# Kernel optimization log

Measured on AMD Instinct MI355X. Metric: run time of the kernel, lower is better.

Reference implementation:

```python
import jax, jax.numpy as jnp
import numpy as np

EMB = 512
HEADS = 8
HEAD_DIM = EMB // HEADS


def setup_inputs() -> dict:
    key = jax.random.key(0)
    ks = jax.random.split(key, 8)
    S, B = 2048, 2
    q = jax.random.normal(ks[0], (S, B, EMB), dtype=jnp.float32)
    k = jax.random.normal(ks[1], (S, B, EMB), dtype=jnp.float32)
    v = jax.random.normal(ks[2], (S, B, EMB), dtype=jnp.float32)
    sc = 1.0 / np.sqrt(HEAD_DIM)
    Wq = jax.random.normal(ks[3], (HEAD_DIM, HEAD_DIM), dtype=jnp.float32) * sc
    Wk = jax.random.normal(ks[4], (HEAD_DIM, HEAD_DIM), dtype=jnp.float32) * sc
    Wv = jax.random.normal(ks[5], (HEAD_DIM, HEAD_DIM), dtype=jnp.float32) * sc
    Wfc = jax.random.normal(ks[6], (EMB, EMB), dtype=jnp.float32) * (1.0 / np.sqrt(EMB))
    bfc = jax.random.normal(ks[7], (EMB,), dtype=jnp.float32) * 0.01
    return {"q": q, "k": k, "v": v, "Wq": Wq, "Wk": Wk, "Wv": Wv, "Wfc": Wfc, "bfc": bfc}


def reference(q, k, v, Wq, Wk, Wv, Wfc, bfc):
    query_len, batch, emb = q.shape
    key_len = k.shape[0]
    value_len = v.shape[0]
    # Faithful to the original: plain reshape (NOT transpose) from [S,B,E] -> [B,H,S,D]
    qh = q.reshape(batch, HEADS, query_len, HEAD_DIM)
    kh = k.reshape(batch, HEADS, key_len, HEAD_DIM)
    vh = v.reshape(batch, HEADS, value_len, HEAD_DIM)
    # torch Linear(head_dim, head_dim, bias=False): y = x @ W.T
    Q = qh @ Wq.T
    K = kh @ Wk.T
    V = vh @ Wv.T
    QK = jnp.einsum('bhqd,bhkd->bhqk', Q, K)  # [B,H,S,S] score matrix (memory-bound)
    filt = jax.nn.softmax(QK / np.sqrt(HEAD_DIM).astype(np.float32), axis=3)
    att = jnp.einsum('bhqk,bhkd->bhqd', filt, V)
    att = att.reshape(query_len, batch, emb)
    return att @ Wfc.T + bfc
```

## Files before the change

kernel.cpp:

```cpp
#include <hip/hip_runtime.h>
#include <hip/hip_bf16.h>


typedef __attribute__((ext_vector_type(8))) __bf16 bf16x8;
typedef __attribute__((ext_vector_type(4))) float f32x4;
typedef __attribute__((ext_vector_type(16))) float f32x16;
typedef __attribute__((ext_vector_type(4))) unsigned short u16x4;
typedef __attribute__((ext_vector_type(4))) unsigned int u32x4;
typedef unsigned short u16;
typedef unsigned int u32;

static __device__ __forceinline__ u16 f2bf(float x) {
    u32 u = __float_as_uint(x);
    u += 0x7fff + ((u >> 16) & 1);
    return (u16)(u >> 16);
}
static __device__ __forceinline__ float bf2f(u16 h) {
    return __uint_as_float(((u32)h) << 16);
}
static __device__ __forceinline__ u32 pk2(float lo, float hi) {
    __hip_bfloat162 h2 = __float22bfloat162_rn(make_float2(lo, hi));
    u32 r; __builtin_memcpy(&r, &h2, 4); return r;
}

__global__ __launch_bounds__(256) void proj_kernel(
    const float* __restrict__ q, const float* __restrict__ k, const float* __restrict__ v,
    const float* __restrict__ Wq, const float* __restrict__ Wk, const float* __restrict__ Wv,
    const float* __restrict__ Wfc,
    u16* __restrict__ Qb, u16* __restrict__ Kb, u16* __restrict__ Vt,
    u16* __restrict__ Wb, float* __restrict__ KnSq)
{
    const int mode = blockIdx.z;
    const int t = threadIdx.x;

    if (mode == 3) {
        int i = (blockIdx.x * 256 + t) * 4;
        float4 val = *(const float4*)(Wfc + i);
        uint2 b = { pk2(val.x, val.y), pk2(val.z, val.w) };
        *(uint2*)(Wb + i) = b;
        return;
    }

    const float* A = (mode == 0) ? q : (mode == 1) ? k : v;
    const float* W = (mode == 0) ? Wq : (mode == 1) ? Wk : Wv;
    const float osc = (mode == 0) ? 0.18033688011112042f : 1.0f;

    __shared__ alignas(16) u16 Ash[128 * 88];
    __shared__ alignas(16) u16 Wsh[64 * 88];
    __shared__ float red[128];

    const int m0 = blockIdx.x * 128;
    const int w = t >> 6, l = t & 63;
    const int r16 = l & 15, q4 = l >> 4;

    {
        const float4* A4 = (const float4*)(A + (size_t)m0 * 64);
        const int c4 = t & 15;
        #pragma unroll
        for (int i = 0; i < 8; ++i) {
            int row = (t >> 4) + i * 16;
            float4 val = A4[row * 16 + c4];
            uint2 bb = { pk2(val.x, val.y), pk2(val.z, val.w) };
            *(uint2*)(Ash + row * 88 + c4 * 4) = bb;
        }
        const float4* W4 = (const float4*)W;
        #pragma unroll
        for (int i = 0; i < 4; ++i) {
            int row = (t >> 4) + i * 16;
            float4 val = W4[row * 16 + c4];
            uint2 bb = { pk2(val.x, val.y), pk2(val.z, val.w) };
            *(uint2*)(Wsh + row * 88 + c4 * 4) = bb;
        }
    }
    __syncthreads();

    bf16x8 af[2][2], wf[4][2];
    #pragma unroll
    for (int mc = 0; mc < 2; ++mc)
        #pragma unroll
        for (int kk = 0; kk < 2; ++kk)
            af[mc][kk] = *(const bf16x8*)(Ash + (w * 32 + mc * 16 + r16) * 88 + kk * 32 + q4 * 8);
    #pragma unroll
    for (int nc = 0; nc < 4; ++nc)
        #pragma unroll
        for (int kk = 0; kk < 2; ++kk)
            wf[nc][kk] = *(const bf16x8*)(Wsh + (nc * 16 + r16) * 88 + kk * 32 + q4 * 8);

    f32x4 acc[2][4];
    const f32x4 zero = {0.f, 0.f, 0.f, 0.f};
    #pragma unroll
    for (int mc = 0; mc < 2; ++mc)
        #pragma unroll
        for (int nc = 0; nc < 4; ++nc) {
            acc[mc][nc] = __builtin_amdgcn_mfma_f32_16x16x32_bf16(af[mc][0], wf[nc][0], zero, 0, 0, 0);
            acc[mc][nc] = __builtin_amdgcn_mfma_f32_16x16x32_bf16(af[mc][1], wf[nc][1], acc[mc][nc], 0, 0, 0);
        }

    __syncthreads();

    if (mode < 2) {
        #pragma unroll
        for (int mc = 0; mc < 2; ++mc)
            #pragma unroll
            for (int nc = 0; nc < 4; ++nc)
                #pragma unroll
                for (int r = 0; r < 4; ++r)
                    Ash[(w * 32 + mc * 16 + q4 * 4 + r) * 72 + nc * 16 + r16] = f2bf(acc[mc][nc][r] * osc);
        __syncthreads();
        u16* Out = ((mode == 0) ? Qb : Kb) + (size_t)m0 * 64;
        {
            int row = t >> 1, cbase = (t & 1) * 32;
            #pragma unroll
            for (int i = 0; i < 4; ++i)
                *(u32x4*)(Out + row * 64 + cbase + i * 8) = *(const u32x4*)(Ash + row * 72 + cbase + i * 8);
        }
        if (mode == 1) {
            if (t < 128) {
                float ss = 0.f;
                #pragma unroll
                for (int c = 0; c < 8; ++c) {
                    u32x4 d = *(const u32x4*)(Ash + t * 72 + c * 8);
                    #pragma unroll
                    for (int j = 0; j < 4; ++j) {
                        float lo = bf2f((u16)(d[j] & 0xffff));
                        float hi = bf2f((u16)(d[j] >> 16));
                        ss += lo * lo + hi * hi;
                    }
                }
                red[t] = ss;
            }
            __syncthreads();
            if (t < 64) red[t] = fmaxf(red[t], red[t + 64]);
            __syncthreads();
            if (t < 32) red[t] = fmaxf(red[t], red[t + 32]);
            __syncthreads();
            if (t == 0) {
                float mx = red[0];
                for (int i = 1; i < 32; ++i) mx = fmaxf(mx, red[i]);
                KnSq[blockIdx.x] = mx;
            }
        }
    } else {
        #pragma unroll
        for (int mc = 0; mc < 2; ++mc)
            #pragma unroll
            for (int nc = 0; nc < 4; ++nc)
                #pragma unroll
                for (int r = 0; r < 4; ++r)
                    Ash[(nc * 16 + r16) * 136 + w * 32 + mc * 16 + q4 * 4 + r] = f2bf(acc[mc][nc][r]);
        __syncthreads();
        const int g = m0 >> 11, s0 = m0 & 2047;
        int d = t >> 2, sb = (t & 3) * 32;
        u16* Out = Vt + ((size_t)(g * 64 + d)) * 2048 + s0;
        #pragma unroll
        for (int i = 0; i < 4; ++i)
            *(u32x4*)(Out + sb + i * 8) = *(const u32x4*)(Ash + d * 136 + sb + i * 8);
    }
}

__global__ __launch_bounds__(256) void flash_kernel(
    const u16* __restrict__ Qb, const u16* __restrict__ Kb,
    const u16* __restrict__ Vt, const float* __restrict__ KnSq,
    u16* __restrict__ Att)
{
    const int bi = blockIdx.x;
    const int g = bi & 15;
    const int qt = bi >> 4;
    const int t = threadIdx.x, w = t >> 6, l = t & 63;
    const int q5 = l & 31, h = l >> 5;
    const int qs = w >> 1, kh = w & 1;

    __shared__ alignas(16) unsigned char smem[43008];
    u16* const base16 = (u16*)smem;
    u16* const KT0 = base16;
    u16* const KT1 = base16 + 4096;
    u16* const VS0 = base16 + 8192;
    u16* const VS1 = base16 + 12288;
    u16* const PwB = base16 + 16384 + w * 1280;

    const u16* Kg = Kb + ((size_t)g) * 2048 * 64;
    const u16* Vg = Vt + ((size_t)g) * 64 * 2048;

    bf16x8 qb[4];
    {
        const u16* qp = Qb + ((size_t)(g * 2048 + qt * 64 + qs * 32 + q5)) * 64;
        #pragma unroll
        for (int s = 0; s < 4; ++s)
            qb[s] = *(const bf16x8*)(qp + s * 16 + h * 8);
    }

    float m;
    {
        float kss = KnSq[g * 16 + (l & 15)];
        kss = fmaxf(kss, __shfl_xor(kss, 1));
        kss = fmaxf(kss, __shfl_xor(kss, 2));
        kss = fmaxf(kss, __shfl_xor(kss, 4));
        kss = fmaxf(kss, __shfl_xor(kss, 8));
        float ss = 0.f;
        #pragma unroll
        for (int s = 0; s < 4; ++s)
            #pragma unroll
            for (int j = 0; j < 8; ++j) {
                float x = (float)qb[s][j];
                ss += x * x;
            }
        ss += __shfl_xor(ss, 32);
        m = sqrtf(ss * kss) * 1.0002f;
    }

    const int rr = t >> 3, ck = t & 7;
    const int sw = (ck ^ (rr & 7)) * 8;

    {
        #pragma unroll
        for (int h2 = 0; h2 < 2; ++h2) {
            int row = h2 * 32 + rr;
            *(u32x4*)(KT0 + row * 64 + sw) = *(const u32x4*)(Kg + (size_t)row * 64 + ck * 8);
            *(u32x4*)(VS0 + row * 64 + sw) = *(const u32x4*)(Vg + (size_t)row * 2048 + ck * 8);
        }
    }
    __syncthreads();

    f32x16 z16;
    #pragma unroll
    for (int r = 0; r < 16; ++r) z16[r] = 0.f;
    f32x16 o0 = z16, o1 = z16;
    float psum = 0.f;

    const int rk = kh * 32 + q5;
    const int r7 = q5 & 7;
    u16* const pwRow = PwB + q5 * 40;
    const int vc0 = 4 * kh + h;
    const int vc1 = 4 * kh + 2 + h;

    for (int it = 0; it < 32; ++it) {
        u16* const KTc = (it & 1) ? KT1 : KT0;
        u16* const VSc = (it & 1) ? VS1 : VS0;
        u16* const KTn = (it & 1) ? KT0 : KT1;
        u16* const VSn = (it & 1) ? VS0 : VS1;
        const bool hasn = (it < 31);

        u32x4 knx[2], vnx[2];
        if (hasn) {
            #pragma unroll
            for (int h2 = 0; h2 < 2; ++h2) {
                int row = h2 * 32 + rr;
                knx[h2] = *(const u32x4*)(Kg + (size_t)((it + 1) * 64 + row) * 64 + ck * 8);
                vnx[h2] = *(const u32x4*)(Vg + (size_t)row * 2048 + (it + 1) * 64 + ck * 8);
            }
        }

        bf16x8 ka0 = *(const bf16x8*)(KTc + rk * 64 + (((0 + h) ^ r7) * 8));
        bf16x8 ka1 = *(const bf16x8*)(KTc + rk * 64 + (((2 + h) ^ r7) * 8));
        bf16x8 ka2 = *(const bf16x8*)(KTc + rk * 64 + (((4 + h) ^ r7) * 8));
        bf16x8 ka3 = *(const bf16x8*)(KTc + rk * 64 + (((6 + h) ^ r7) * 8));
        f32x16 s;
        s = __builtin_amdgcn_mfma_f32_32x32x16_bf16(ka0, qb[0], z16, 0, 0, 0);
        s = __builtin_amdgcn_mfma_f32_32x32x16_bf16(ka1, qb[1], s, 0, 0, 0);
        s = __builtin_amdgcn_mfma_f32_32x32x16_bf16(ka2, qb[2], s, 0, 0, 0);
        s = __builtin_amdgcn_mfma_f32_32x32x16_bf16(ka3, qb[3], s, 0, 0, 0);

        float p[16];
        float ps = 0.f;
        #pragma unroll
        for (int r = 0; r < 16; ++r) {
            p[r] = exp2f(s[r] - m);
            ps += p[r];
        }
        psum += ps;

        #pragma unroll
        for (int u = 0; u < 4; ++u) {
            uint2 dd = { pk2(p[4 * u + 0], p[4 * u + 1]),
                         pk2(p[4 * u + 2], p[4 * u + 3]) };
            *(uint2*)(pwRow + u * 8 + 4 * h) = dd;
        }
        bf16x8 pb0 = *(const bf16x8*)(pwRow + (0 + h) * 8);
        bf16x8 pb1 = *(const bf16x8*)(pwRow + (2 + h) * 8);

        {
            bf16x8 va0 = *(const bf16x8*)(VSc + q5 * 64 + ((vc0 ^ r7) * 8));
            bf16x8 va1 = *(const bf16x8*)(VSc + q5 * 64 + ((vc1 ^ r7) * 8));
            o0 = __builtin_amdgcn_mfma_f32_32x32x16_bf16(va0, pb0, o0, 0, 0, 0);
            o0 = __builtin_amdgcn_mfma_f32_32x32x16_bf16(va1, pb1, o0, 0, 0, 0);
        }
        {
            bf16x8 va0 = *(const bf16x8*)(VSc + (32 + q5) * 64 + ((vc0 ^ r7) * 8));
            bf16x8 va1 = *(const bf16x8*)(VSc + (32 + q5) * 64 + ((vc1 ^ r7) * 8));
            o1 = __builtin_amdgcn_mfma_f32_32x32x16_bf16(va0, pb0, o1, 0, 0, 0);
            o1 = __builtin_amdgcn_mfma_f32_32x32x16_bf16(va1, pb1, o1, 0, 0, 0);
        }

        if (hasn) {
            #pragma unroll
            for (int h2 = 0; h2 < 2; ++h2) {
                int row = h2 * 32 + rr;
                *(u32x4*)(KTn + row * 64 + sw) = knx[h2];
                *(u32x4*)(VSn + row * 64 + sw) = vnx[h2];
            }
        }
        __syncthreads();
    }

    float psq = psum + __shfl_xor(psum, 32);

    float* const Fsh = (float*)smem;
    float* const LsF = (float*)(smem + 16896);
    u16*  const Osh = (u16*)(smem + 18432);

    if (kh == 1) {
        float* fp = Fsh + (qs * 64 + l) * 33;
        #pragma unroll
        for (int r = 0; r < 16; ++r) { fp[r] = o0[r]; fp[16 + r] = o1[r]; }
        fp[32] = psq;
        LsF[qs * 64 + l] = psq;
    }
    __syncthreads();
    if (kh == 0) {
        const float* fp = Fsh + (qs * 64 + l) * 33;
        float inv = 1.0f / (psq + LsF[qs * 64 + l]);
        const int qloc = qs * 32 + q5;
        #pragma unroll
        for (int u = 0; u < 4; ++u) {
            uint2 b0 = { pk2((o0[4*u+0] + fp[4*u+0]) * inv, (o0[4*u+1] + fp[4*u+1]) * inv),
                         pk2((o0[4*u+2] + fp[4*u+2]) * inv, (o0[4*u+3] + fp[4*u+3]) * inv) };
            *(uint2*)(Osh + qloc * 72 + 8 * u + 4 * h) = b0;
            uint2 b1 = { pk2((o1[4*u+0] + fp[16+4*u+0]) * inv, (o1[4*u+1] + fp[16+4*u+1]) * inv),
                         pk2((o1[4*u+2] + fp[16+4*u+2]) * inv, (o1[4*u+3] + fp[16+4*u+3]) * inv) };
            *(uint2*)(Osh + qloc * 72 + 32 + 8 * u + 4 * h) = b1;
        }
    }
    __syncthreads();
    {
        int row = t >> 2, cb = (t & 3) * 16;
        u16* dst = Att + ((size_t)(g * 2048 + qt * 64 + row)) * 64 + cb;
        *(u32x4*)(dst)     = *(const u32x4*)(Osh + row * 72 + cb);
        *(u32x4*)(dst + 8) = *(const u32x4*)(Osh + row * 72 + cb + 8);
    }
}

__global__ __launch_bounds__(256) void fc_kernel(
    const u16* __restrict__ Att, const u16* __restrict__ Wb,
    const float* __restrict__ bfc, float* __restrict__ out)
{
    __shared__ alignas(16) u16 Ash[2][64 * 64];
    __shared__ alignas(16) u16 Wsh[2][64 * 64];

    const int t = threadIdx.x, w = t >> 6, l = t & 63;
    const int r16 = l & 15, q4 = l >> 4;
    const int r7 = r16 & 7;
    const int m0 = blockIdx.x * 64, n0 = blockIdx.y * 64;

    const int rr = t >> 3, ck = t & 7;
    const int sw0 = (ck ^ (rr & 7)) * 8;
    const int fr0 = (q4 ^ r7) * 8;
    const int fr1 = ((q4 + 4) ^ r7) * 8;

    {
        #pragma unroll
        for (int h = 0; h < 2; ++h) {
            int row = h * 32 + rr;
            *(u32x4*)(&Ash[0][row * 64 + sw0]) = *(const u32x4*)(Att + (size_t)(m0 + row) * 512 + ck * 8);
            *(u32x4*)(&Wsh[0][row * 64 + sw0]) = *(const u32x4*)(Wb + (size_t)(n0 + row) * 512 + ck * 8);
        }
    }
    __syncthreads();

    f32x4 acc[4];
    const f32x4 zero = {0.f, 0.f, 0.f, 0.f};
    #pragma unroll
    for (int nc = 0; nc < 4; ++nc) acc[nc] = zero;

    for (int it = 0; it < 8; ++it) {
        const int cur = it & 1;
        const bool hasn = (it < 7);

        u32x4 anx[2], wnx[2];
        if (hasn) {
            #pragma unroll
            for (int h = 0; h < 2; ++h) {
                int row = h * 32 + rr;
                anx[h] = *(const u32x4*)(Att + (size_t)(m0 + row) * 512 + (it + 1) * 64 + ck * 8);
                wnx[h] = *(const u32x4*)(Wb + (size_t)(n0 + row) * 512 + (it + 1) * 64 + ck * 8);
            }
        }

        bf16x8 af[2], wf[4][2];
        af[0] = *(const bf16x8*)(&Ash[cur][(w * 16 + r16) * 64 + fr0]);
        af[1] = *(const bf16x8*)(&Ash[cur][(w * 16 + r16) * 64 + fr1]);
        #pragma unroll
        for (int nc = 0; nc < 4; ++nc) {
            wf[nc][0] = *(const bf16x8*)(&Wsh[cur][(nc * 16 + r16) * 64 + fr0]);
            wf[nc][1] = *(const bf16x8*)(&Wsh[cur][(nc * 16 + r16) * 64 + fr1]);
        }

        #pragma unroll
        for (int nc = 0; nc < 4; ++nc) {
            acc[nc] = __builtin_amdgcn_mfma_f32_16x16x32_bf16(af[0], wf[nc][0], acc[nc], 0, 0, 0);
            acc[nc] = __builtin_amdgcn_mfma_f32_16x16x32_bf16(af[1], wf[nc][1], acc[nc], 0, 0, 0);
        }

        if (hasn) {
            const int nxt = cur ^ 1;
            #pragma unroll
            for (int h = 0; h < 2; ++h) {
                int row = h * 32 + rr;
                *(u32x4*)(&Ash[nxt][row * 64 + sw0]) = anx[h];
                *(u32x4*)(&Wsh[nxt][row * 64 + sw0]) = wnx[h];
            }
        }
        __syncthreads();
    }

    #pragma unroll
    for (int nc = 0; nc < 4; ++nc) {
        float bb = bfc[n0 + nc * 16 + r16];
        #pragma unroll
        for (int r = 0; r < 4; ++r) {
            int row = m0 + w * 16 + q4 * 4 + r;
            out[(size_t)row * 512 + n0 + nc * 16 + r16] = acc[nc][r] + bb;
        }
    }
}

extern "C" void kernel_launch(void* const* d_in, const int* in_sizes, int n_in,
                              void* d_out, int out_size, void* d_ws, size_t ws_size,
                              hipStream_t stream) {
    (void)in_sizes; (void)n_in; (void)out_size; (void)ws_size;
    const float* q   = (const float*)d_in[0];
    const float* k   = (const float*)d_in[1];
    const float* v   = (const float*)d_in[2];
    const float* Wq  = (const float*)d_in[3];
    const float* Wk  = (const float*)d_in[4];
    const float* Wv  = (const float*)d_in[5];
    const float* Wfc = (const float*)d_in[6];
    const float* bfc = (const float*)d_in[7];
    float* out = (float*)d_out;

    u16* Qb = (u16*)d_ws;
    u16* Kb = Qb + 2097152;
    u16* Vt = Kb + 2097152;
    u16* At = Vt + 2097152;
    u16* Wb = At + 2097152;
    float* KnSq = (float*)((char*)d_ws + 17301504);

    proj_kernel<<<dim3(256, 1, 4), 256, 0, stream>>>(q, k, v, Wq, Wk, Wv, Wfc,
                                                     Qb, Kb, Vt, Wb, KnSq);
    flash_kernel<<<dim3(512), 256, 0, stream>>>(Qb, Kb, Vt, KnSq, At);
    fc_kernel<<<dim3(64, 8), 256, 0, stream>>>(At, Wb, bfc, out);
}
```

Before: 138.3 us.

## Store Q/K/V in MFMA fragment layout and load K/V directly into registers

The projection kernel now writes Q, K and V in a pre-swizzled layout that matches the MFMA operand fragments. This lets the flash kernel load K/V tiles straight from global memory into registers with register double-buffering, removing the LDS staging and the per-iteration __syncthreads. It also folds the -m offset into the MFMA accumulator init and computes the row sum with an extra MFMA against a ones vector instead of scalar adds. In exchange, each wave redundantly fetches K/V from global/L2 instead of sharing them through LDS, and it uses more registers.

```diff
diff --git a/kernel.cpp b/kernel.cpp
--- a/kernel.cpp
+++ b/kernel.cpp
@@ -27,7 +27,7 @@
     const float* __restrict__ q, const float* __restrict__ k, const float* __restrict__ v,
     const float* __restrict__ Wq, const float* __restrict__ Wk, const float* __restrict__ Wv,
     const float* __restrict__ Wfc,
-    u16* __restrict__ Qb, u16* __restrict__ Kb, u16* __restrict__ Vt,
+    u16* __restrict__ Qf, u16* __restrict__ Kf, u16* __restrict__ Vf,
     u16* __restrict__ Wb, float* __restrict__ KnSq)
 {
     const int mode = blockIdx.z;
@@ -97,6 +97,8 @@
         }
 
     __syncthreads();
+
+    const int g = m0 >> 11, t0 = (m0 & 2047) >> 6;
 
     if (mode < 2) {
         #pragma unroll
@@ -107,12 +109,17 @@
                 for (int r = 0; r < 4; ++r)
                     Ash[(w * 32 + mc * 16 + q4 * 4 + r) * 72 + nc * 16 + r16] = f2bf(acc[mc][nc][r] * osc);
         __syncthreads();
-        u16* Out = ((mode == 0) ? Qb : Kb) + (size_t)m0 * 64;
-        {
-            int row = t >> 1, cbase = (t & 1) * 32;
-            #pragma unroll
-            for (int i = 0; i < 4; ++i)
-                *(u32x4*)(Out + row * 64 + cbase + i * 8) = *(const u32x4*)(Ash + row * 72 + cbase + i * 8);
+        u16* Out = (mode == 0) ? Qf : Kf;
+        #pragma unroll
+        for (int i = 0; i < 4; ++i) {
+            int idx = i * 256 + t;
+            int ll = idx & 63;
+            int r = idx >> 6;
+            int tl = r >> 3, c2 = (r >> 2) & 1, s = r & 3;
+            int row = tl * 64 + c2 * 32 + (ll & 31);
+            int col = s * 16 + (ll >> 5) * 8;
+            u32x4 d = *(const u32x4*)(Ash + row * 72 + col);
+            *(u32x4*)(Out + ((size_t)(((g * 32 + t0 + tl) * 2 + c2) * 4 + s) * 64 + ll) * 8) = d;
         }
         if (mode == 1) {
             if (t < 128) {
@@ -149,18 +156,23 @@
                 for (int r = 0; r < 4; ++r)
                     Ash[(nc * 16 + r16) * 136 + w * 32 + mc * 16 + q4 * 4 + r] = f2bf(acc[mc][nc][r]);
         __syncthreads();
-        const int g = m0 >> 11, s0 = m0 & 2047;
-        int d = t >> 2, sb = (t & 3) * 32;
-        u16* Out = Vt + ((size_t)(g * 64 + d)) * 2048 + s0;
-        #pragma unroll
-        for (int i = 0; i < 4; ++i)
-            *(u32x4*)(Out + sb + i * 8) = *(const u32x4*)(Ash + d * 136 + sb + i * 8);
+        #pragma unroll
+        for (int i = 0; i < 4; ++i) {
+            int idx = i * 256 + t;
+            int ll = idx & 63;
+            int r = idx >> 6;
+            int tl = r >> 3, kh = (r >> 2) & 1, dc = (r >> 1) & 1, s2 = r & 1;
+            int d = dc * 32 + (ll & 31);
+            int keycol = tl * 64 + kh * 32 + s2 * 16 + (ll >> 5) * 8;
+            u32x4 val = *(const u32x4*)(Ash + d * 136 + keycol);
+            *(u32x4*)(Vf + ((size_t)((((g * 32 + t0 + tl) * 2 + kh) * 2 + dc) * 2 + s2) * 64 + ll) * 8) = val;
+        }
     }
 }
 
 __global__ __launch_bounds__(256) void flash_kernel(
-    const u16* __restrict__ Qb, const u16* __restrict__ Kb,
-    const u16* __restrict__ Vt, const float* __restrict__ KnSq,
+    const u16* __restrict__ Qf, const u16* __restrict__ Kf,
+    const u16* __restrict__ Vf, const float* __restrict__ KnSq,
     u16* __restrict__ Att)
 {
     const int bi = blockIdx.x;
@@ -170,24 +182,16 @@
     const int q5 = l & 31, h = l >> 5;
     const int qs = w >> 1, kh = w & 1;
 
-    __shared__ alignas(16) unsigned char smem[43008];
-    u16* const base16 = (u16*)smem;
-    u16* const KT0 = base16;
-    u16* const KT1 = base16 + 4096;
-    u16* const VS0 = base16 + 8192;
-    u16* const VS1 = base16 + 12288;
-    u16* const PwB = base16 + 16384 + w * 1280;
-
-    const u16* Kg = Kb + ((size_t)g) * 2048 * 64;
-    const u16* Vg = Vt + ((size_t)g) * 64 * 2048;
+    __shared__ alignas(16) unsigned char smem[26624];
+    u16* const pwRow = (u16*)smem + w * 1280 + q5 * 40;
+
+    const u16* qbase = Qf + ((size_t)(((g * 32 + qt) * 2 + qs) * 4)) * 512 + l * 8;
+    const u16* kbase = Kf + ((size_t)((g * 32 * 2 + kh) * 4)) * 512 + l * 8;
+    const u16* vbase = Vf + ((size_t)((g * 32 * 2 + kh) * 4)) * 512 + l * 8;
 
     bf16x8 qb[4];
-    {
-        const u16* qp = Qb + ((size_t)(g * 2048 + qt * 64 + qs * 32 + q5)) * 64;
-        #pragma unroll
-        for (int s = 0; s < 4; ++s)
-            qb[s] = *(const bf16x8*)(qp + s * 16 + h * 8);
-    }
+    #pragma unroll
+    for (int s = 0; s < 4; ++s) qb[s] = *(const bf16x8*)(qbase + s * 512);
 
     float m;
     {
@@ -208,66 +212,37 @@
         m = sqrtf(ss * kss) * 1.0002f;
     }
 
-    const int rr = t >> 3, ck = t & 7;
-    const int sw = (ck ^ (rr & 7)) * 8;
-
-    {
-        #pragma unroll
-        for (int h2 = 0; h2 < 2; ++h2) {
-            int row = h2 * 32 + rr;
-            *(u32x4*)(KT0 + row * 64 + sw) = *(const u32x4*)(Kg + (size_t)row * 64 + ck * 8);
-            *(u32x4*)(VS0 + row * 64 + sw) = *(const u32x4*)(Vg + (size_t)row * 2048 + ck * 8);
-        }
-    }
-    __syncthreads();
-
-    f32x16 z16;
-    #pragma unroll
-    for (int r = 0; r < 16; ++r) z16[r] = 0.f;
-    f32x16 o0 = z16, o1 = z16;
-    float psum = 0.f;
-
-    const int rk = kh * 32 + q5;
-    const int r7 = q5 & 7;
-    u16* const pwRow = PwB + q5 * 40;
-    const int vc0 = 4 * kh + h;
-    const int vc1 = 4 * kh + 2 + h;
+    f32x16 mC, o0, o1, ol;
+    #pragma unroll
+    for (int r = 0; r < 16; ++r) { mC[r] = -m; o0[r] = 0.f; o1[r] = 0.f; ol[r] = 0.f; }
+
+    const u16 one_bf = 0x3F80;
+    bf16x8 ones;
+    #pragma unroll
+    for (int j = 0; j < 8; ++j) ones[j] = ((const __bf16*)&one_bf)[0];
+
+    bf16x8 ka[4], va[4], kan[4], van[4];
+    #pragma unroll
+    for (int s = 0; s < 4; ++s) ka[s] = *(const bf16x8*)(kbase + s * 512);
+    #pragma unroll
+    for (int j = 0; j < 4; ++j) va[j] = *(const bf16x8*)(vbase + j * 512);
 
     for (int it = 0; it < 32; ++it) {
-        u16* const KTc = (it & 1) ? KT1 : KT0;
-        u16* const VSc = (it & 1) ? VS1 : VS0;
-        u16* const KTn = (it & 1) ? KT0 : KT1;
-        u16* const VSn = (it & 1) ? VS0 : VS1;
-        const bool hasn = (it < 31);
-
-        u32x4 knx[2], vnx[2];
-        if (hasn) {
-            #pragma unroll
-            for (int h2 = 0; h2 < 2; ++h2) {
-                int row = h2 * 32 + rr;
-                knx[h2] = *(const u32x4*)(Kg + (size_t)((it + 1) * 64 + row) * 64 + ck * 8);
-                vnx[h2] = *(const u32x4*)(Vg + (size_t)row * 2048 + (it + 1) * 64 + ck * 8);
-            }
-        }
-
-        bf16x8 ka0 = *(const bf16x8*)(KTc + rk * 64 + (((0 + h) ^ r7) * 8));
-        bf16x8 ka1 = *(const bf16x8*)(KTc + rk * 64 + (((2 + h) ^ r7) * 8));
-        bf16x8 ka2 = *(const bf16x8*)(KTc + rk * 64 + (((4 + h) ^ r7) * 8));
-        bf16x8 ka3 = *(const bf16x8*)(KTc + rk * 64 + (((6 + h) ^ r7) * 8));
+        const size_t nx = (size_t)((it + 1) & 31) * 4096;
+        #pragma unroll
+        for (int s = 0; s < 4; ++s) kan[s] = *(const bf16x8*)(kbase + nx + s * 512);
+        #pragma unroll
+        for (int j = 0; j < 4; ++j) van[j] = *(const bf16x8*)(vbase + nx + j * 512);
+
         f32x16 s;
-        s = __builtin_amdgcn_mfma_f32_32x32x16_bf16(ka0, qb[0], z16, 0, 0, 0);
-        s = __builtin_amdgcn_mfma_f32_32x32x16_bf16(ka1, qb[1], s, 0, 0, 0);
-        s = __builtin_amdgcn_mfma_f32_32x32x16_bf16(ka2, qb[2], s, 0, 0, 0);
-        s = __builtin_amdgcn_mfma_f32_32x32x16_bf16(ka3, qb[3], s, 0, 0, 0);
+        s = __builtin_amdgcn_mfma_f32_32x32x16_bf16(ka[0], qb[0], mC, 0, 0, 0);
+        s = __builtin_amdgcn_mfma_f32_32x32x16_bf16(ka[1], qb[1], s, 0, 0, 0);
+        s = __builtin_amdgcn_mfma_f32_32x32x16_bf16(ka[2], qb[2], s, 0, 0, 0);
+        s = __builtin_amdgcn_mfma_f32_32x32x16_bf16(ka[3], qb[3], s, 0, 0, 0);
 
         float p[16];
-        float ps = 0.f;
-        #pragma unroll
-        for (int r = 0; r < 16; ++r) {
-            p[r] = exp2f(s[r] - m);
-            ps += p[r];
-        }
-        psum += ps;
+        #pragma unroll
+        for (int r = 0; r < 16; ++r) p[r] = exp2f(s[r]);
 
         #pragma unroll
         for (int u = 0; u < 4; ++u) {
@@ -278,36 +253,24 @@
         bf16x8 pb0 = *(const bf16x8*)(pwRow + (0 + h) * 8);
         bf16x8 pb1 = *(const bf16x8*)(pwRow + (2 + h) * 8);
 
-        {
-            bf16x8 va0 = *(const bf16x8*)(VSc + q5 * 64 + ((vc0 ^ r7) * 8));
-            bf16x8 va1 = *(const bf16x8*)(VSc + q5 * 64 + ((vc1 ^ r7) * 8));
-            o0 = __builtin_amdgcn_mfma_f32_32x32x16_bf16(va0, pb0, o0, 0, 0, 0);
-            o0 = __builtin_amdgcn_mfma_f32_32x32x16_bf16(va1, pb1, o0, 0, 0, 0);
-        }
-        {
-            bf16x8 va0 = *(const bf16x8*)(VSc + (32 + q5) * 64 + ((vc0 ^ r7) * 8));
-            bf16x8 va1 = *(const bf16x8*)(VSc + (32 + q5) * 64 + ((vc1 ^ r7) * 8));
-            o1 = __builtin_amdgcn_mfma_f32_32x32x16_bf16(va0, pb0, o1, 0, 0, 0);
-            o1 = __builtin_amdgcn_mfma_f32_32x32x16_bf16(va1, pb1, o1, 0, 0, 0);
-        }
-
-        if (hasn) {
-            #pragma unroll
-            for (int h2 = 0; h2 < 2; ++h2) {
-                int row = h2 * 32 + rr;
-                *(u32x4*)(KTn + row * 64 + sw) = knx[h2];
-                *(u32x4*)(VSn + row * 64 + sw) = vnx[h2];
-            }
-        }
-        __syncthreads();
-    }
-
-    float psq = psum + __shfl_xor(psum, 32);
+        o0 = __builtin_amdgcn_mfma_f32_32x32x16_bf16(va[0], pb0, o0, 0, 0, 0);
+        o0 = __builtin_amdgcn_mfma_f32_32x32x16_bf16(va[1], pb1, o0, 0, 0, 0);
+        o1 = __builtin_amdgcn_mfma_f32_32x32x16_bf16(va[2], pb0, o1, 0, 0, 0);
+        o1 = __builtin_amdgcn_mfma_f32_32x32x16_bf16(va[3], pb1, o1, 0, 0, 0);
+        ol = __builtin_amdgcn_mfma_f32_32x32x16_bf16(ones, pb0, ol, 0, 0, 0);
+        ol = __builtin_amdgcn_mfma_f32_32x32x16_bf16(ones, pb1, ol, 0, 0, 0);
+
+        #pragma unroll
+        for (int s2 = 0; s2 < 4; ++s2) { ka[s2] = kan[s2]; va[s2] = van[s2]; }
+    }
+
+    float psq = ol[0];
 
     float* const Fsh = (float*)smem;
     float* const LsF = (float*)(smem + 16896);
-    u16*  const Osh = (u16*)(smem + 18432);
-
+    u16*  const Osh = (u16*)(smem + 17408);
+
+    __syncthreads();
     if (kh == 1) {
         float* fp = Fsh + (qs * 64 + l) * 33;
         #pragma unroll
@@ -437,15 +400,15 @@
     const float* bfc = (const float*)d_in[7];
     float* out = (float*)d_out;
 
-    u16* Qb = (u16*)d_ws;
-    u16* Kb = Qb + 2097152;
-    u16* Vt = Kb + 2097152;
-    u16* At = Vt + 2097152;
+    u16* Qf = (u16*)d_ws;
+    u16* Kf = Qf + 2097152;
+    u16* Vf = Kf + 2097152;
+    u16* At = Vf + 2097152;
     u16* Wb = At + 2097152;
     float* KnSq = (float*)((char*)d_ws + 17301504);
 
     proj_kernel<<<dim3(256, 1, 4), 256, 0, stream>>>(q, k, v, Wq, Wk, Wv, Wfc,
-                                                     Qb, Kb, Vt, Wb, KnSq);
-    flash_kernel<<<dim3(512), 256, 0, stream>>>(Qb, Kb, Vt, KnSq, At);
+                                                     Qf, Kf, Vf, Wb, KnSq);
+    flash_kernel<<<dim3(512), 256, 0, stream>>>(Qf, Kf, Vf, KnSq, At);
     fc_kernel<<<dim3(64, 8), 256, 0, stream>>>(At, Wb, bfc, out);
 }
```

After: 128.2 us. 1.08x faster.
